# Optimization experiments

Measured on AMD Instinct MI355X. Metric: run time of the kernel, lower is better.

Reference implementation:

```python
import jax, jax.numpy as jnp
import numpy as np


def setup_inputs() -> dict:
    key = jax.random.key(0)
    k = jax.random.split(key, 6)
    B, S, d, n = 4, 4096, 1024, 64
    x = jax.random.normal(k[0], (B, S, d), dtype=jnp.float32)
    gate_W = jax.random.normal(k[1], (d, n), dtype=jnp.float32) / np.sqrt(d).astype(np.float32)
    gate_b = jnp.full((n,), 3.0, dtype=jnp.float32)  # nn.init.constant_(gate_proj.bias, 3.0)
    B_W = jax.random.normal(k[2], (d, n), dtype=jnp.float32) / np.sqrt(d).astype(np.float32)
    C_W = jax.random.normal(k[3], (n, d), dtype=jnp.float32) / np.sqrt(n).astype(np.float32)
    out_W = jax.random.normal(k[4], (d, d), dtype=jnp.float32) / np.sqrt(d).astype(np.float32)
    mix_weight = jnp.eye(n, dtype=jnp.float32) + 0.01 * jax.random.normal(k[5], (n, n), dtype=jnp.float32)
    return {"x": x, "gate_W": gate_W, "gate_b": gate_b, "B_W": B_W,
            "C_W": C_W, "out_W": out_W, "mix_weight": mix_weight, "chunk_size": 16}


def _ssm_forward(x, gate_W, gate_b, B_W, C_W, out_W, mix_weight, chunk_size):
    Bb, S, d = x.shape
    n = gate_W.shape[1]
    C = chunk_size
    K = S // C  # seq_len chosen divisible by chunk_size -> F.pad path is a no-op
    # Vectorized per-timestep projections (done once for the whole sequence)
    gates = jax.nn.sigmoid(jnp.einsum('bsd,dn->bsn', x, gate_W) + gate_b)  # a_t in (0,1)
    b_all = jnp.einsum('bsd,dn->bsn', x, B_W)
    a_ch = gates.reshape(Bb, K, C, n).transpose(1, 2, 0, 3)  # (K, C, B, n)
    b_ch = b_all.reshape(Bb, K, C, n).transpose(1, 2, 0, 3)

    def chunk_step(h_prev, ab):
        a_c, b_c = ab  # each (C, B, n)
        def step(h, t):
            a_t, b_t = t
            h = a_t * h + b_t
            return h, h
        h_final, h_stack = jax.lax.scan(step, h_prev, (a_c, b_c))  # h_stack: (C, B, n)
        gate_prod = jnp.prod(a_c, axis=0)  # (B, n) cumulative diag gates
        # T_chunk = mix @ diag(gate_prod): T[b,i,j] = mix[i,j] * gate_prod[b,j]
        T = mix_weight[None, :, :] * gate_prod[:, None, :]
        Th = jnp.einsum('bij,bj->bi', T, h_prev)
        b_chunk = h_final - Th
        h_next = Th + b_chunk  # canonical inter-chunk propagation: T @ h_prev + b_chunk
        return h_next, h_stack

    h0 = jnp.zeros((Bb, n), dtype=x.dtype)
    _, h_all = jax.lax.scan(chunk_step, h0, (a_ch, b_ch))  # (K, C, B, n)
    h_seq = h_all.transpose(2, 0, 1, 3).reshape(Bb, S, n)
    y = jnp.einsum('bsn,nd->bsd', h_seq, C_W)
    out_gate = jax.nn.sigmoid(jnp.einsum('bsd,de->bse', x, out_W))
    return y * out_gate


def reference(x, gate_W, gate_b, B_W, C_W, out_W, mix_weight, chunk_size):
    return _ssm_forward(x, gate_W, gate_b, B_W, C_W, out_W, mix_weight, chunk_size)
```

## Files before the change

kernel.cpp:

```cpp
#include <hip/hip_runtime.h>
#include <stdint.h>

typedef __attribute__((ext_vector_type(8))) short short8;
typedef __attribute__((ext_vector_type(4))) float f32x4;
typedef __attribute__((ext_vector_type(4))) float f4;
typedef __attribute__((ext_vector_type(4))) unsigned short us4;

typedef unsigned short ushort_t;

__device__ __forceinline__ ushort_t f2bf(float f) {
    union { float f; uint32_t u; } c; c.f = f;
    uint32_t u = c.u;
    uint32_t r = u + 0x7fffu + ((u >> 16) & 1u);
    return (ushort_t)(r >> 16);
}
__device__ __forceinline__ float bf2f(ushort_t h) {
    union { uint32_t u; float f; } c; c.u = ((uint32_t)h) << 16;
    return c.f;
}

typedef const __attribute__((address_space(1))) unsigned int as1_uint;
typedef __attribute__((address_space(3))) unsigned int as3_uint;
__device__ __forceinline__ void gload_lds16(const void* g, void* l) {
    __builtin_amdgcn_global_load_lds((as1_uint*)g, (as3_uint*)l, 16, 0, 0);
}

#define SWIDX(r, c) ((r) * 64 + ((c) ^ (((r) & 7) << 3)))

__global__ void prep_weights(const float* __restrict__ gate_W, const float* __restrict__ B_W,
                             const float* __restrict__ C_W, const float* __restrict__ out_W,
                             ushort_t* __restrict__ W1t_hi, ushort_t* __restrict__ W1t_lo,
                             ushort_t* __restrict__ outWt, ushort_t* __restrict__ Ct)
{
    int idx = blockIdx.x * 256 + threadIdx.x;
    int stride = gridDim.x * 256;
    for (int i = idx; i < 1024 * 1024; i += stride) {
        int nn = i >> 10, kk = i & 1023;
        outWt[i] = f2bf(out_W[kk * 1024 + nn]);
    }
    for (int i = idx; i < 128 * 1024; i += stride) {
        int nn = i >> 10, kk = i & 1023;
        float v = (nn < 64) ? gate_W[kk * 64 + nn] : B_W[kk * 64 + (nn - 64)];
        ushort_t h = f2bf(v);
        W1t_hi[i] = h;
        W1t_lo[i] = f2bf(v - bf2f(h));
    }
    for (int i = idx; i < 1024 * 64; i += stride) {
        int nn = i >> 6, kk = i & 63;
        Ct[i] = f2bf(C_W[kk * 1024 + nn]);
    }
}

__global__ __launch_bounds__(256, 2)
void p1_kernel(const float* __restrict__ x,
               const ushort_t* __restrict__ W1t_hi, const ushort_t* __restrict__ W1t_lo,
               ushort_t* __restrict__ x_hi, float* __restrict__ Zpart)
{
    __shared__ ushort_t Ash[128 * 64];
    __shared__ ushort_t Asl[128 * 64];
    __shared__ ushort_t Bsh[64 * 64];

    const int tid = threadIdx.x;
    const int wave = tid >> 6, lane = tid & 63;
    const int wm = wave >> 1, wn = wave & 1;
    const int s0 = blockIdx.x * 64;
    const int kc = blockIdx.y;

    f32x4 acc[4][2];
#pragma unroll
    for (int i = 0; i < 4; i++)
#pragma unroll
        for (int j = 0; j < 2; j++) { f32x4 z = {0.f,0.f,0.f,0.f}; acc[i][j] = z; }

    for (int kt = 0; kt < 8; ++kt) {
        const int k0 = kc * 512 + kt * 64;
#pragma unroll
        for (int p = 0; p < 4; ++p) {
            int c = p * 256 + wave * 64 + lane;
            int row = c >> 3, col = (c & 7) * 8;
            gload_lds16(W1t_hi + (size_t)row * 1024 + k0 + col,
                        &Ash[(p * 256 + wave * 64) * 8]);
            gload_lds16(W1t_lo + (size_t)row * 1024 + k0 + col,
                        &Asl[(p * 256 + wave * 64) * 8]);
        }
#pragma unroll
        for (int p = 0; p < 4; ++p) {
            int f = tid + p * 256;
            int row = f >> 4, col = (f & 15) * 4;
            f4 v = *(const f4*)(x + (size_t)(s0 + row) * 1024 + k0 + col);
            us4 hi;
#pragma unroll
            for (int j = 0; j < 4; j++) hi[j] = f2bf(v[j]);
            *(us4*)&Bsh[row * 64 + col] = hi;
            *(us4*)(x_hi + (size_t)(s0 + row) * 1024 + k0 + col) = hi;
        }
        __syncthreads();
#pragma unroll
        for (int kk = 0; kk < 2; ++kk) {
            const int kb = kk * 32 + (lane >> 4) * 8;
            short8 ah[4], al[4], bh[2];
#pragma unroll
            for (int fm = 0; fm < 4; fm++) {
                int r = wm * 64 + fm * 16 + (lane & 15);
                ah[fm] = *(const short8*)&Ash[r * 64 + kb];
                al[fm] = *(const short8*)&Asl[r * 64 + kb];
            }
#pragma unroll
            for (int fn = 0; fn < 2; fn++) {
                int r = wn * 32 + fn * 16 + (lane & 15);
                bh[fn] = *(const short8*)&Bsh[r * 64 + kb];
            }
#pragma unroll
            for (int fm = 0; fm < 4; fm++)
#pragma unroll
                for (int fn = 0; fn < 2; fn++) {
                    acc[fm][fn] = __builtin_amdgcn_mfma_f32_16x16x32_bf16(ah[fm], bh[fn], acc[fm][fn], 0, 0, 0);
                    acc[fm][fn] = __builtin_amdgcn_mfma_f32_16x16x32_bf16(al[fm], bh[fn], acc[fm][fn], 0, 0, 0);
                }
        }
        __syncthreads();
    }
#pragma unroll
    for (int fm = 0; fm < 4; fm++) {
#pragma unroll
        for (int fn = 0; fn < 2; fn++) {
            int scol = s0 + wn * 32 + fn * 16 + (lane & 15);
            int b = scol >> 12, sb = scol & 4095;
            int nbase = wm * 64 + fm * 16 + ((lane >> 4) << 2);
#pragma unroll
            for (int r = 0; r < 4; r++) {
                Zpart[((size_t)kc * 512 + b * 128 + nbase + r) * 4096 + sb] = acc[fm][fn][r];
            }
        }
    }
}

__global__ __launch_bounds__(256)
void scan_kernel(const float* __restrict__ Zpart, const float* __restrict__ gate_b,
                 ushort_t* __restrict__ hT)
{
    __shared__ float SA[256], SB[256];
    const int bn = blockIdx.x;
    const int t = threadIdx.x;
    const int b = bn >> 6, n = bn & 63;
    const float gb = gate_b[n];
    const float* g0 = Zpart + ((size_t)(b * 128 + n)) * 4096;
    const float* g1 = g0 + (size_t)512 * 4096;
    const float* b0 = Zpart + ((size_t)(b * 128 + 64 + n)) * 4096;
    const float* b1 = b0 + (size_t)512 * 4096;
    const int sb = t * 16;

    float a[16], bb[16];
#pragma unroll
    for (int q = 0; q < 4; q++) {
        f4 vg0 = *(const f4*)(g0 + sb + q * 4);
        f4 vg1 = *(const f4*)(g1 + sb + q * 4);
        f4 vb0 = *(const f4*)(b0 + sb + q * 4);
        f4 vb1 = *(const f4*)(b1 + sb + q * 4);
#pragma unroll
        for (int j = 0; j < 4; j++) {
            a[q * 4 + j] = 1.f / (1.f + __expf(-(vg0[j] + vg1[j] + gb)));
            bb[q * 4 + j] = vb0[j] + vb1[j];
        }
    }
    float A = 1.f, Bv = 0.f;
#pragma unroll
    for (int i = 0; i < 16; i++) { Bv = a[i] * Bv + bb[i]; A *= a[i]; }
    SA[t] = A; SB[t] = Bv;
    __syncthreads();
    for (int off = 1; off < 256; off <<= 1) {
        float a1 = 1.f, b1v = 0.f;
        if (t >= off) { a1 = SA[t - off]; b1v = SB[t - off]; }
        float a2 = SA[t], b2 = SB[t];
        __syncthreads();
        SA[t] = a1 * a2;
        SB[t] = a2 * b1v + b2;
        __syncthreads();
    }
    float h = (t == 0) ? 0.f : SB[t - 1];
    ushort_t ov[16];
#pragma unroll
    for (int i = 0; i < 16; i++) {
        h = a[i] * h + bb[i];
        ov[i] = f2bf(h);
    }
    ushort_t* dst = hT + (size_t)bn * 4096 + sb;
#pragma unroll
    for (int q = 0; q < 4; q++) {
        us4 o; o[0]=ov[q*4]; o[1]=ov[q*4+1]; o[2]=ov[q*4+2]; o[3]=ov[q*4+3];
        *(us4*)(dst + q * 4) = o;
    }
}

__global__ __launch_bounds__(512, 2)
void gemm_out256(const ushort_t* __restrict__ x_hi, const ushort_t* __restrict__ outWt,
                 const ushort_t* __restrict__ hT, const ushort_t* __restrict__ Ct,
                 float* __restrict__ out)
{
    __shared__ ushort_t As[2][256 * 64];
    __shared__ ushort_t Bs[2][256 * 64];

    const int tid = threadIdx.x;
    const int wave = tid >> 6, lane = tid & 63;
    const int wm = wave >> 2;
    const int wn = wave & 3;

    const int flat = blockIdx.x;
    const int swz = (flat & 7) * 32 + (flat >> 3);
    const int m0 = (swz >> 2) * 256;
    const int n0 = (swz & 3) * 256;

    const int lcol0 = (lane >> 4) * 8;
    const int lrow = lane & 15;
    const int lxor = (lrow & 7) << 3;

    const int aOff0 = (wm * 32 + lrow) * 64 + (lcol0 ^ lxor);
    const int aOff1 = (wm * 32 + lrow) * 64 + ((32 + lcol0) ^ lxor);
    const int bOff0 = (wn * 64 + lrow) * 64 + (lcol0 ^ lxor);
    const int bOff1 = (wn * 64 + lrow) * 64 + ((32 + lcol0) ^ lxor);

    const int rl0 = tid >> 3;
    const int col0 = ((tid & 7) ^ (rl0 & 7)) << 3;
    const ushort_t* gB0a = outWt + (size_t)(n0 + rl0) * 1024 + col0;
    const ushort_t* gB0b = gB0a + 64 * 1024;
    const ushort_t* gB1a = outWt + (size_t)(n0 + 128 + rl0) * 1024 + col0;
    const ushort_t* gB1b = gB1a + 64 * 1024;
    const ushort_t* gA0a = x_hi + (size_t)(m0 + rl0) * 1024 + col0;
    const ushort_t* gA0b = gA0a + 64 * 1024;
    const ushort_t* gA1a = x_hi + (size_t)(m0 + 128 + rl0) * 1024 + col0;
    const ushort_t* gA1b = gA1a + 64 * 1024;

    auto STG = [&](const ushort_t*& ga, const ushort_t*& gb, ushort_t* ldsbase) {
        gload_lds16(ga, ldsbase + wave * 512);
        gload_lds16(gb, ldsbase + 4096 + wave * 512);
        ga += 64; gb += 64;
    };

    f32x4 acc[8][4];
#pragma unroll
    for (int i = 0; i < 8; i++)
#pragma unroll
        for (int j = 0; j < 4; j++) { f32x4 z = {0.f,0.f,0.f,0.f}; acc[i][j] = z; }

    STG(gB0a, gB0b, &Bs[0][0]);
    STG(gB1a, gB1b, &Bs[0][8192]);
    STG(gA0a, gA0b, &As[0][0]);
    STG(gA1a, gA1b, &As[0][8192]);
    asm volatile("s_waitcnt vmcnt(2)" ::: "memory");
    __builtin_amdgcn_s_barrier();

    short8 aR0[2][2], aR1[2][2], bfr[4][2];
#pragma unroll
    for (int mm = 0; mm < 2; ++mm) {
        aR0[mm][0] = *(const short8*)&As[0][aOff0 + mm * 1024];
        aR0[mm][1] = *(const short8*)&As[0][aOff1 + mm * 1024];
    }

#define MFMA_Q(q, AR)                                                              \
    do {                                                                           \
        __builtin_amdgcn_s_setprio(1);                                             \
        _Pragma("unroll") for (int mm = 0; mm < 2; ++mm)                           \
            _Pragma("unroll") for (int fn = 0; fn < 4; ++fn) {                     \
                acc[2*(q)+mm][fn] = __builtin_amdgcn_mfma_f32_16x16x32_bf16(       \
                    AR[mm][0], bfr[fn][0], acc[2*(q)+mm][fn], 0, 0, 0);            \
                acc[2*(q)+mm][fn] = __builtin_amdgcn_mfma_f32_16x16x32_bf16(       \
                    AR[mm][1], bfr[fn][1], acc[2*(q)+mm][fn], 0, 0, 0);            \
            }                                                                      \
        __builtin_amdgcn_s_setprio(0);                                             \
    } while (0)

    for (int t = 0; t < 16; ++t) {
        const int bc = t & 1;
        const ushort_t* as = &As[bc][0];
        const ushort_t* bs = &Bs[bc][0];
        const ushort_t* asn = &As[bc ^ 1][0];

        if (t < 15) STG(gB0a, gB0b, &Bs[bc ^ 1][0]);
#pragma unroll
        for (int fn = 0; fn < 4; ++fn) {
            bfr[fn][0] = *(const short8*)(bs + bOff0 + fn * 1024);
            bfr[fn][1] = *(const short8*)(bs + bOff1 + fn * 1024);
        }
#pragma unroll
        for (int mm = 0; mm < 2; ++mm) {
            aR1[mm][0] = *(const short8*)(as + aOff0 + 4096 + mm * 1024);
            aR1[mm][1] = *(const short8*)(as + aOff1 + 4096 + mm * 1024);
        }
        asm volatile("s_waitcnt lgkmcnt(4)" ::: "memory");
        __builtin_amdgcn_sched_barrier(0);
        MFMA_Q(0, aR0);
        if (t < 15) { asm volatile("s_waitcnt vmcnt(2)" ::: "memory"); }
        else        { asm volatile("s_waitcnt vmcnt(0)" ::: "memory"); }
        __builtin_amdgcn_s_barrier();

        if (t < 15) {
            STG(gB1a, gB1b, &Bs[bc ^ 1][8192]);
            STG(gA0a, gA0b, &As[bc ^ 1][0]);
        }
#pragma unroll
        for (int mm = 0; mm < 2; ++mm) {
            aR0[mm][0] = *(const short8*)(as + aOff0 + 2 * 4096 + mm * 1024);
            aR0[mm][1] = *(const short8*)(as + aOff1 + 2 * 4096 + mm * 1024);
        }
        asm volatile("s_waitcnt lgkmcnt(4)" ::: "memory");
        __builtin_amdgcn_sched_barrier(0);
        MFMA_Q(1, aR1);
        __builtin_amdgcn_s_barrier();

        if (t < 15) STG(gA1a, gA1b, &As[bc ^ 1][8192]);
#pragma unroll
        for (int mm = 0; mm < 2; ++mm) {
            aR1[mm][0] = *(const short8*)(as + aOff0 + 3 * 4096 + mm * 1024);
            aR1[mm][1] = *(const short8*)(as + aOff1 + 3 * 4096 + mm * 1024);
        }
        asm volatile("s_waitcnt lgkmcnt(4)" ::: "memory");
        __builtin_amdgcn_sched_barrier(0);
        MFMA_Q(2, aR0);
        if (t < 15) { asm volatile("s_waitcnt vmcnt(2)" ::: "memory"); }
        __builtin_amdgcn_s_barrier();

        if (t < 15) {
#pragma unroll
            for (int mm = 0; mm < 2; ++mm) {
                aR0[mm][0] = *(const short8*)(asn + aOff0 + mm * 1024);
                aR0[mm][1] = *(const short8*)(asn + aOff1 + mm * 1024);
            }
            asm volatile("s_waitcnt lgkmcnt(4)" ::: "memory");
        } else {
            asm volatile("s_waitcnt lgkmcnt(0)" ::: "memory");
        }
        __builtin_amdgcn_sched_barrier(0);
        MFMA_Q(3, aR1);
        __builtin_amdgcn_s_barrier();
    }
#undef MFMA_Q

    const int b64 = (m0 >> 12) * 64;
    const int sb0 = m0 & 4095;
#pragma unroll
    for (int p = 0; p < 4; ++p) {
        int c = p * 512 + wave * 64 + lane;
        int row = c >> 3;
        int col = (((c & 7) ^ (row & 7)) << 3);
        gload_lds16(Ct + (size_t)(n0 + row) * 64 + col,
                    &Bs[0][(p * 512 + wave * 64) * 8]);
    }
#pragma unroll
    for (int p = 0; p < 4; ++p) {
        int c = tid + p * 512;
        int kn = c & 63, mc = c >> 6;
        short8 v = *(const short8*)(hT + (size_t)(b64 + kn) * 4096 + sb0 + mc * 8);
#pragma unroll
        for (int j = 0; j < 8; ++j)
            As[0][SWIDX(mc * 8 + j, kn)] = (ushort_t)v[j];
    }
    __syncthreads();

    short8 by[4][2];
#pragma unroll
    for (int fn = 0; fn < 4; fn++)
#pragma unroll
        for (int kk = 0; kk < 2; kk++) {
            int r = wn * 64 + fn * 16 + lrow;
            by[fn][kk] = *(const short8*)&Bs[0][SWIDX(r, kk * 32 + lcol0)];
        }

#pragma unroll
    for (int g = 0; g < 4; g++) {
        f32x4 ty[2][4];
#pragma unroll
        for (int mm = 0; mm < 2; mm++)
#pragma unroll
            for (int fn = 0; fn < 4; fn++) { f32x4 z = {0.f,0.f,0.f,0.f}; ty[mm][fn] = z; }
#pragma unroll
        for (int mm = 0; mm < 2; mm++) {
            int r = g * 64 + wm * 32 + mm * 16 + lrow;
            short8 a0 = *(const short8*)&As[0][SWIDX(r, lcol0)];
            short8 a1 = *(const short8*)&As[0][SWIDX(r, 32 + lcol0)];
#pragma unroll
            for (int fn = 0; fn < 4; fn++) {
                ty[mm][fn] = __builtin_amdgcn_mfma_f32_16x16x32_bf16(a0, by[fn][0], ty[mm][fn], 0, 0, 0);
                ty[mm][fn] = __builtin_amdgcn_mfma_f32_16x16x32_bf16(a1, by[fn][1], ty[mm][fn], 0, 0, 0);
            }
        }
#pragma unroll
        for (int mm = 0; mm < 2; mm++)
#pragma unroll
            for (int fn = 0; fn < 4; fn++) {
                int col = n0 + wn * 64 + fn * 16 + lrow;
                int rbase = m0 + g * 64 + wm * 32 + mm * 16 + ((lane >> 4) << 2);
#pragma unroll
                for (int r = 0; r < 4; r++) {
                    float og = 1.f / (1.f + __expf(-acc[g * 2 + mm][fn][r]));
                    out[(size_t)(rbase + r) * 1024 + col] = ty[mm][fn][r] * og;
                }
            }
    }
}

extern "C" void kernel_launch(void* const* d_in, const int* in_sizes, int n_in,
                              void* d_out, int out_size, void* d_ws, size_t ws_size,
                              hipStream_t stream)
{
    const float* x      = (const float*)d_in[0];
    const float* gate_W = (const float*)d_in[1];
    const float* gate_b = (const float*)d_in[2];
    const float* B_W    = (const float*)d_in[3];
    const float* C_W    = (const float*)d_in[4];
    const float* out_W  = (const float*)d_in[5];
    float* out = (float*)d_out;

    char* ws = (char*)d_ws;
    float*    Zpart  = (float*)(ws + 0);
    ushort_t* hT     = (ushort_t*)(ws + 16777216);
    ushort_t* x_hi   = (ushort_t*)(ws + 18874368);
    ushort_t* W1t_hi = (ushort_t*)(ws + 52428800);
    ushort_t* W1t_lo = (ushort_t*)(ws + 52690944);
    ushort_t* outWt  = (ushort_t*)(ws + 52953088);
    ushort_t* Ct     = (ushort_t*)(ws + 55050240);

    prep_weights<<<512, 256, 0, stream>>>(gate_W, B_W, C_W, out_W,
                                          W1t_hi, W1t_lo, outWt, Ct);

    p1_kernel<<<dim3(256, 2), 256, 0, stream>>>(x, W1t_hi, W1t_lo, x_hi, Zpart);

    scan_kernel<<<256, 256, 0, stream>>>(Zpart, gate_b, hT);

    gemm_out256<<<256, 512, 0, stream>>>(x_hi, outWt, hT, Ct, out);
}
```

Measured before the change: 83.95 us.

## Use 4-wave blocks with 32x128 per-wave tiles in output GEMM

```diff
diff --git a/kernel.cpp b/kernel.cpp
--- a/kernel.cpp
+++ b/kernel.cpp
@@ -192,8 +192,8 @@
     }
 }
 
-__global__ __launch_bounds__(512, 2)
-void gemm_out256(const ushort_t* __restrict__ x_hi, const ushort_t* __restrict__ outWt,
+__global__ __launch_bounds__(256, 1)
+void gemm_fat256(const ushort_t* __restrict__ x_hi, const ushort_t* __restrict__ outWt,
                  const ushort_t* __restrict__ hT, const ushort_t* __restrict__ Ct,
                  float* __restrict__ out)
 {
@@ -202,8 +202,8 @@
 
     const int tid = threadIdx.x;
     const int wave = tid >> 6, lane = tid & 63;
-    const int wm = wave >> 2;
-    const int wn = wave & 3;
+    const int wm = wave >> 1;
+    const int wn = wave & 1;
 
     const int flat = blockIdx.x;
     const int swz = (flat & 7) * 32 + (flat >> 3);
@@ -216,40 +216,37 @@
 
     const int aOff0 = (wm * 32 + lrow) * 64 + (lcol0 ^ lxor);
     const int aOff1 = (wm * 32 + lrow) * 64 + ((32 + lcol0) ^ lxor);
-    const int bOff0 = (wn * 64 + lrow) * 64 + (lcol0 ^ lxor);
-    const int bOff1 = (wn * 64 + lrow) * 64 + ((32 + lcol0) ^ lxor);
+    const int bOff0 = (wn * 128 + lrow) * 64 + (lcol0 ^ lxor);
+    const int bOff1 = (wn * 128 + lrow) * 64 + ((32 + lcol0) ^ lxor);
 
     const int rl0 = tid >> 3;
     const int col0 = ((tid & 7) ^ (rl0 & 7)) << 3;
-    const ushort_t* gB0a = outWt + (size_t)(n0 + rl0) * 1024 + col0;
-    const ushort_t* gB0b = gB0a + 64 * 1024;
-    const ushort_t* gB1a = outWt + (size_t)(n0 + 128 + rl0) * 1024 + col0;
-    const ushort_t* gB1b = gB1a + 64 * 1024;
-    const ushort_t* gA0a = x_hi + (size_t)(m0 + rl0) * 1024 + col0;
-    const ushort_t* gA0b = gA0a + 64 * 1024;
-    const ushort_t* gA1a = x_hi + (size_t)(m0 + 128 + rl0) * 1024 + col0;
-    const ushort_t* gA1b = gA1a + 64 * 1024;
-
-    auto STG = [&](const ushort_t*& ga, const ushort_t*& gb, ushort_t* ldsbase) {
-        gload_lds16(ga, ldsbase + wave * 512);
-        gload_lds16(gb, ldsbase + 4096 + wave * 512);
-        ga += 64; gb += 64;
+    const ushort_t* gB0 = outWt + (size_t)(n0 + rl0) * 1024 + col0;
+    const ushort_t* gB1 = outWt + (size_t)(n0 + 128 + rl0) * 1024 + col0;
+    const ushort_t* gA0 = x_hi + (size_t)(m0 + rl0) * 1024 + col0;
+    const ushort_t* gA1 = x_hi + (size_t)(m0 + 128 + rl0) * 1024 + col0;
+
+    auto STG = [&](const ushort_t*& g, ushort_t* ldsbase) {
+#pragma unroll
+        for (int i = 0; i < 4; ++i)
+            gload_lds16(g + (size_t)i * 32 * 1024, ldsbase + i * 2048 + wave * 512);
+        g += 64;
     };
 
-    f32x4 acc[8][4];
+    f32x4 acc[8][8];
 #pragma unroll
     for (int i = 0; i < 8; i++)
 #pragma unroll
-        for (int j = 0; j < 4; j++) { f32x4 z = {0.f,0.f,0.f,0.f}; acc[i][j] = z; }
-
-    STG(gB0a, gB0b, &Bs[0][0]);
-    STG(gB1a, gB1b, &Bs[0][8192]);
-    STG(gA0a, gA0b, &As[0][0]);
-    STG(gA1a, gA1b, &As[0][8192]);
-    asm volatile("s_waitcnt vmcnt(2)" ::: "memory");
+        for (int j = 0; j < 8; j++) { f32x4 z = {0.f,0.f,0.f,0.f}; acc[i][j] = z; }
+
+    STG(gB0, &Bs[0][0]);
+    STG(gB1, &Bs[0][8192]);
+    STG(gA0, &As[0][0]);
+    STG(gA1, &As[0][8192]);
+    asm volatile("s_waitcnt vmcnt(4)" ::: "memory");
     __builtin_amdgcn_s_barrier();
 
-    short8 aR0[2][2], aR1[2][2], bfr[4][2];
+    short8 aR0[2][2], aR1[2][2], bfr[8][2];
 #pragma unroll
     for (int mm = 0; mm < 2; ++mm) {
         aR0[mm][0] = *(const short8*)&As[0][aOff0 + mm * 1024];
@@ -260,7 +257,7 @@
     do {                                                                           \
         __builtin_amdgcn_s_setprio(1);                                             \
         _Pragma("unroll") for (int mm = 0; mm < 2; ++mm)                           \
-            _Pragma("unroll") for (int fn = 0; fn < 4; ++fn) {                     \
+            _Pragma("unroll") for (int fn = 0; fn < 8; ++fn) {                     \
                 acc[2*(q)+mm][fn] = __builtin_amdgcn_mfma_f32_16x16x32_bf16(       \
                     AR[mm][0], bfr[fn][0], acc[2*(q)+mm][fn], 0, 0, 0);            \
                 acc[2*(q)+mm][fn] = __builtin_amdgcn_mfma_f32_16x16x32_bf16(       \
@@ -275,9 +272,9 @@
         const ushort_t* bs = &Bs[bc][0];
         const ushort_t* asn = &As[bc ^ 1][0];
 
-        if (t < 15) STG(gB0a, gB0b, &Bs[bc ^ 1][0]);
-#pragma unroll
-        for (int fn = 0; fn < 4; ++fn) {
+        if (t < 15) STG(gB0, &Bs[bc ^ 1][0]);
+#pragma unroll
+        for (int fn = 0; fn < 8; ++fn) {
             bfr[fn][0] = *(const short8*)(bs + bOff0 + fn * 1024);
             bfr[fn][1] = *(const short8*)(bs + bOff1 + fn * 1024);
         }
@@ -289,13 +286,13 @@
         asm volatile("s_waitcnt lgkmcnt(4)" ::: "memory");
         __builtin_amdgcn_sched_barrier(0);
         MFMA_Q(0, aR0);
-        if (t < 15) { asm volatile("s_waitcnt vmcnt(2)" ::: "memory"); }
+        if (t < 15) { asm volatile("s_waitcnt vmcnt(4)" ::: "memory"); }
         else        { asm volatile("s_waitcnt vmcnt(0)" ::: "memory"); }
         __builtin_amdgcn_s_barrier();
 
         if (t < 15) {
-            STG(gB1a, gB1b, &Bs[bc ^ 1][8192]);
-            STG(gA0a, gA0b, &As[bc ^ 1][0]);
+            STG(gB1, &Bs[bc ^ 1][8192]);
+            STG(gA0, &As[bc ^ 1][0]);
         }
 #pragma unroll
         for (int mm = 0; mm < 2; ++mm) {
@@ -307,7 +304,7 @@
         MFMA_Q(1, aR1);
         __builtin_amdgcn_s_barrier();
 
-        if (t < 15) STG(gA1a, gA1b, &As[bc ^ 1][8192]);
+        if (t < 15) STG(gA1, &As[bc ^ 1][8192]);
 #pragma unroll
         for (int mm = 0; mm < 2; ++mm) {
             aR1[mm][0] = *(const short8*)(as + aOff0 + 3 * 4096 + mm * 1024);
@@ -316,7 +313,7 @@
         asm volatile("s_waitcnt lgkmcnt(4)" ::: "memory");
         __builtin_amdgcn_sched_barrier(0);
         MFMA_Q(2, aR0);
-        if (t < 15) { asm volatile("s_waitcnt vmcnt(2)" ::: "memory"); }
+        if (t < 15) { asm volatile("s_waitcnt vmcnt(4)" ::: "memory"); }
         __builtin_amdgcn_s_barrier();
 
         if (t < 15) {
@@ -338,16 +335,16 @@
     const int b64 = (m0 >> 12) * 64;
     const int sb0 = m0 & 4095;
 #pragma unroll
-    for (int p = 0; p < 4; ++p) {
-        int c = p * 512 + wave * 64 + lane;
+    for (int p = 0; p < 8; ++p) {
+        int c = tid + p * 256;
         int row = c >> 3;
         int col = (((c & 7) ^ (row & 7)) << 3);
         gload_lds16(Ct + (size_t)(n0 + row) * 64 + col,
-                    &Bs[0][(p * 512 + wave * 64) * 8]);
-    }
-#pragma unroll
-    for (int p = 0; p < 4; ++p) {
-        int c = tid + p * 512;
+                    &Bs[0][p * 2048 + wave * 512]);
+    }
+#pragma unroll
+    for (int p = 0; p < 8; ++p) {
+        int c = tid + p * 256;
         int kn = c & 63, mc = c >> 6;
         short8 v = *(const short8*)(hT + (size_t)(b64 + kn) * 4096 + sb0 + mc * 8);
 #pragma unroll
@@ -356,29 +353,27 @@
     }
     __syncthreads();
 
-    short8 by[4][2];
-#pragma unroll
-    for (int fn = 0; fn < 4; fn++)
-#pragma unroll
-        for (int kk = 0; kk < 2; kk++) {
-            int r = wn * 64 + fn * 16 + lrow;
-            by[fn][kk] = *(const short8*)&Bs[0][SWIDX(r, kk * 32 + lcol0)];
-        }
+    short8 by[8][2];
+#pragma unroll
+    for (int fn = 0; fn < 8; fn++) {
+        by[fn][0] = *(const short8*)&Bs[0][bOff0 + fn * 1024];
+        by[fn][1] = *(const short8*)&Bs[0][bOff1 + fn * 1024];
+    }
 
 #pragma unroll
     for (int g = 0; g < 4; g++) {
-        f32x4 ty[2][4];
+        f32x4 ty[2][8];
 #pragma unroll
         for (int mm = 0; mm < 2; mm++)
 #pragma unroll
-            for (int fn = 0; fn < 4; fn++) { f32x4 z = {0.f,0.f,0.f,0.f}; ty[mm][fn] = z; }
+            for (int fn = 0; fn < 8; fn++) { f32x4 z = {0.f,0.f,0.f,0.f}; ty[mm][fn] = z; }
 #pragma unroll
         for (int mm = 0; mm < 2; mm++) {
             int r = g * 64 + wm * 32 + mm * 16 + lrow;
             short8 a0 = *(const short8*)&As[0][SWIDX(r, lcol0)];
             short8 a1 = *(const short8*)&As[0][SWIDX(r, 32 + lcol0)];
 #pragma unroll
-            for (int fn = 0; fn < 4; fn++) {
+            for (int fn = 0; fn < 8; fn++) {
                 ty[mm][fn] = __builtin_amdgcn_mfma_f32_16x16x32_bf16(a0, by[fn][0], ty[mm][fn], 0, 0, 0);
                 ty[mm][fn] = __builtin_amdgcn_mfma_f32_16x16x32_bf16(a1, by[fn][1], ty[mm][fn], 0, 0, 0);
             }
@@ -386,8 +381,8 @@
 #pragma unroll
         for (int mm = 0; mm < 2; mm++)
 #pragma unroll
-            for (int fn = 0; fn < 4; fn++) {
-                int col = n0 + wn * 64 + fn * 16 + lrow;
+            for (int fn = 0; fn < 8; fn++) {
+                int col = n0 + wn * 128 + fn * 16 + lrow;
                 int rbase = m0 + g * 64 + wm * 32 + mm * 16 + ((lane >> 4) << 2);
 #pragma unroll
                 for (int r = 0; r < 4; r++) {
@@ -426,5 +421,5 @@
 
     scan_kernel<<<256, 256, 0, stream>>>(Zpart, gate_b, hT);
 
-    gemm_out256<<<256, 512, 0, stream>>>(x_hi, outWt, hT, Ct, out);
-}
+    gemm_fat256<<<256, 256, 0, stream>>>(x_hi, outWt, hT, Ct, out);
+}
```

Result: slower. 89.92 us (+7.1%).
